# Performance work log

Hardware: AMD Instinct MI355X
Metric: run time of the kernel (lower is better)

Reference implementation:

```python
import jax, jax.numpy as jnp
import numpy as np

EMBED_DIM = 1024
NUM_HEADS = 16
HEAD_DIM = EMBED_DIM // NUM_HEADS
WINDOW = 256
B, S = 2, 2048


def setup_inputs() -> dict:
    key = jax.random.key(0)
    ks = jax.random.split(key, 9)
    sc = 1.0 / np.sqrt(EMBED_DIM)
    inp = {
        "x": jax.random.normal(ks[0], (B, S, EMBED_DIM), dtype=jnp.float32),
        "Wq": jax.random.normal(ks[1], (EMBED_DIM, EMBED_DIM), dtype=jnp.float32) * sc,
        "Wk": jax.random.normal(ks[2], (EMBED_DIM, EMBED_DIM), dtype=jnp.float32) * sc,
        "Wv": jax.random.normal(ks[3], (EMBED_DIM, EMBED_DIM), dtype=jnp.float32) * sc,
        "Wo": jax.random.normal(ks[4], (EMBED_DIM, EMBED_DIM), dtype=jnp.float32) * sc,
        "bq": jax.random.normal(ks[5], (EMBED_DIM,), dtype=jnp.float32) * 0.01,
        "bk": jax.random.normal(ks[6], (EMBED_DIM,), dtype=jnp.float32) * 0.01,
        "bv": jax.random.normal(ks[7], (EMBED_DIM,), dtype=jnp.float32) * 0.01,
        "bo": jax.random.normal(ks[8], (EMBED_DIM,), dtype=jnp.float32) * 0.01,
    }
    return inp


def _sliding_window_mask(seq_len: int) -> jnp.ndarray:
    # True where attention is NOT permitted (future or beyond window)
    idx = jnp.arange(seq_len)
    rel = idx[None, :] - idx[:, None]  # (S, S): key_pos - query_pos
    return (rel > 0) | (rel < -WINDOW)


def reference(x, Wq, Wk, Wv, Wo, bq, bk, bv, bo):
    Bx, Sx, E = x.shape
    H, D = NUM_HEADS, HEAD_DIM
    # projections (torch Linear: y = x @ W.T + b)
    q = (x @ Wq.T + bq).reshape(Bx, Sx, H, D).transpose(0, 2, 1, 3)  # (B,H,S,D)
    k = (x @ Wk.T + bk).reshape(Bx, Sx, H, D).transpose(0, 2, 1, 3)
    v = (x @ Wv.T + bv).reshape(Bx, Sx, H, D).transpose(0, 2, 1, 3)
    q = q * (D ** -0.5)
    attn = jnp.einsum("bhqd,bhkd->bhqk", q, k)  # (B,H,S,S) dense scores
    mask = _sliding_window_mask(Sx)
    attn = jnp.where(mask, -jnp.inf, attn)
    attn = jax.nn.softmax(attn, axis=-1)
    y = jnp.einsum("bhqk,bhkd->bhqd", attn, v)
    y = y.transpose(0, 2, 1, 3).reshape(Bx, Sx, E)
    return y @ Wo.T + bo
```

## Files before the change

kernel.cpp:

```cpp
#include <hip/hip_runtime.h>

#define E_DIM 1024
#define NHEAD 16
#define HDIM 64
#define SEQ 2048
#define NBATCH 2
#define WIN 256
#define MTOK (NBATCH * SEQ)
#define BKT 32
#define NT (E_DIM / BKT)

typedef __attribute__((ext_vector_type(4))) float f32x4;
typedef __attribute__((ext_vector_type(8))) short short8;
typedef __attribute__((ext_vector_type(4))) unsigned short u16x4;

#define AS1 __attribute__((address_space(1)))
#define AS3 __attribute__((address_space(3)))

__device__ __forceinline__ void gll16(const void* g, void* l) {
    __builtin_amdgcn_global_load_lds((const AS1 void*)g, (AS3 void*)l, 16, 0, 0);
}

__device__ __forceinline__ unsigned short f2bf(float f) {
    union { float f; unsigned u; } a; a.f = f;
    unsigned r = a.u + 0x7fffu + ((a.u >> 16) & 1u);
    return (unsigned short)(r >> 16);
}

__global__ __launch_bounds__(256) void conv_all(const float* __restrict__ x,
        const float* __restrict__ w0, const float* __restrict__ w1,
        const float* __restrict__ w2, const float* __restrict__ w3,
        unsigned short* __restrict__ xo,
        unsigned short* __restrict__ o0, unsigned short* __restrict__ o1,
        unsigned short* __restrict__ o2, unsigned short* __restrict__ o3) {
    const int seg = blockIdx.y;
    const float* src;
    unsigned short* dst;
    if (seg < 4) { src = x + (size_t)seg * 1048576; dst = xo + (size_t)seg * 1048576; }
    else {
        src = (seg == 4) ? w0 : (seg == 5) ? w1 : (seg == 6) ? w2 : w3;
        dst = (seg == 4) ? o0 : (seg == 5) ? o1 : (seg == 6) ? o2 : o3;
    }
    int i = blockIdx.x * 256 + threadIdx.x;
    float4 v = ((const float4*)src)[i];
    u16x4 o;
    o[0] = f2bf(v.x); o[1] = f2bf(v.y); o[2] = f2bf(v.z); o[3] = f2bf(v.w);
    ((u16x4*)dst)[i] = o;
}

__global__ __launch_bounds__(512, 2) void gemm8_qkv(const unsigned short* __restrict__ xb,
        const unsigned short* __restrict__ wqb, const unsigned short* __restrict__ wkb,
        const unsigned short* __restrict__ wvb,
        const float* __restrict__ bq, const float* __restrict__ bk, const float* __restrict__ bv,
        unsigned short* __restrict__ qo, unsigned short* __restrict__ ko,
        unsigned short* __restrict__ vTo) {
    __shared__ char lds[131072];
    const int tid = threadIdx.x;
    const int w = tid >> 6, l = tid & 63;
    const int r16 = l & 15, kq = l >> 4;
    const int wm = w >> 2, wn = w & 3;
    const int m0 = blockIdx.x * 256;
    const int by = blockIdx.y;
    const int mat = by >> 2;
    const int nb = (by & 3) * 256;
    const unsigned short* Bw = (mat == 0) ? wqb : (mat == 1) ? wkb : wvb;

    const int srow = tid >> 2;
    const int sslot = tid & 3;
    const int fsw = (srow >> 1) & 3;
    const int gslot = (sslot ^ fsw) * 8;
    const unsigned short* aSrc0 = xb + (size_t)(m0 + srow) * E_DIM + gslot;
    const unsigned short* aSrc1 = aSrc0 + (size_t)128 * E_DIM;
    const unsigned short* bSrc0 = Bw + (size_t)(nb + srow) * E_DIM + gslot;
    const unsigned short* bSrc1 = bSrc0 + (size_t)128 * E_DIM;
    const int dstOff = w * 1024;

#define STAGE_A(t) { char* d_ = lds + ((t) & 3) * 32768 + dstOff; \
                     gll16(aSrc0 + (t) * BKT, d_); gll16(aSrc1 + (t) * BKT, d_ + 8192); }
#define STAGE_B(t) { char* d_ = lds + ((t) & 3) * 32768 + 16384 + dstOff; \
                     gll16(bSrc0 + (t) * BKT, d_); gll16(bSrc1 + (t) * BKT, d_ + 8192); }

    f32x4 acc[8][4];
    #pragma unroll
    for (int m = 0; m < 8; ++m)
        #pragma unroll
        for (int n = 0; n < 4; ++n)
            acc[m][n] = (f32x4){0.f, 0.f, 0.f, 0.f};

    STAGE_A(0); STAGE_B(0); STAGE_A(1); STAGE_B(1);

    const int fs = (r16 >> 1) & 3;
    const int rdoff = (kq ^ fs) * 16;

    for (int t = 0; t < NT; ++t) {
        if (t < NT - 1) { asm volatile("s_waitcnt vmcnt(4)" ::: "memory"); }
        else            { asm volatile("s_waitcnt vmcnt(0)" ::: "memory"); }
        __builtin_amdgcn_sched_barrier(0);
        __builtin_amdgcn_s_barrier();
        __builtin_amdgcn_sched_barrier(0);
        char* la = lds + (t & 3) * 32768;
        char* lb = la + 16384;
        short8 bfr[4], af[8];
        #pragma unroll
        for (int n = 0; n < 4; ++n)
            bfr[n] = *(const short8*)(lb + (wn * 64 + n * 16 + r16) * 64 + rdoff);
        #pragma unroll
        for (int j = 0; j < 8; ++j)
            af[j] = *(const short8*)(la + (wm * 128 + j * 16 + r16) * 64 + rdoff);
        if (t + 2 < NT) { STAGE_A(t + 2); STAGE_B(t + 2); }
        __builtin_amdgcn_s_setprio(1);
        #pragma unroll
        for (int j = 0; j < 8; ++j)
            #pragma unroll
            for (int n = 0; n < 4; ++n)
                acc[j][n] = __builtin_amdgcn_mfma_f32_16x16x32_bf16(af[j], bfr[n], acc[j][n], 0, 0, 0);
        __builtin_amdgcn_s_setprio(0);
    }
#undef STAGE_A
#undef STAGE_B

    const float* bias = (mat == 0) ? bq : (mat == 1) ? bk : bv;
    const float scale = (mat == 0) ? 0.125f : 1.0f;
    #pragma unroll
    for (int n = 0; n < 4; ++n) {
        int e = nb + wn * 64 + n * 16 + r16;
        float bb = bias[e];
        int h = e >> 6, d = e & 63;
        #pragma unroll
        for (int m = 0; m < 8; ++m) {
            int tok = m0 + wm * 128 + m * 16 + kq * 4;
            int b = tok >> 11, s = tok & (SEQ - 1);
            if (mat == 2) {
                u16x4 o;
                #pragma unroll
                for (int r = 0; r < 4; ++r) o[r] = f2bf(acc[m][n][r] + bb);
                *(u16x4*)(vTo + ((size_t)(b * NHEAD + h) * HDIM + d) * SEQ + s) = o;
            } else {
                unsigned short* dst = (mat == 0) ? qo : ko;
                #pragma unroll
                for (int r = 0; r < 4; ++r) {
                    float val = (acc[m][n][r] + bb) * scale;
                    dst[((size_t)(b * NHEAD + h) * SEQ + s + r) * HDIM + d] = f2bf(val);
                }
            }
        }
    }
}

__global__ __launch_bounds__(256, 2) void gemm_out(const unsigned short* __restrict__ yb,
        const unsigned short* __restrict__ wob, const float* __restrict__ bo,
        float* __restrict__ out) {
    __shared__ char lds[65536];
    const int tid = threadIdx.x;
    const int w = tid >> 6, l = tid & 63;
    const int r16 = l & 15, kq = l >> 4;
    const int wr = w >> 1, wc = w & 1;
    const int m0 = blockIdx.x * 128;
    const int n0 = blockIdx.y * 128;

    const int srow = tid >> 2;
    const int sslot = tid & 3;
    const int fsw = (srow >> 1) & 3;
    const int gslot = (sslot ^ fsw) * 8;
    const unsigned short* aSrc0 = yb + (size_t)(m0 + srow) * E_DIM + gslot;
    const unsigned short* aSrc1 = aSrc0 + (size_t)64 * E_DIM;
    const unsigned short* bSrc0 = wob + (size_t)(n0 + srow) * E_DIM + gslot;
    const unsigned short* bSrc1 = bSrc0 + (size_t)64 * E_DIM;
    const int dstOff = w * 1024;

#define STAGE_A(t) { char* d_ = lds + ((t) & 3) * 16384 + dstOff; \
                     gll16(aSrc0 + (t) * BKT, d_); gll16(aSrc1 + (t) * BKT, d_ + 4096); }
#define STAGE_B(t) { char* d_ = lds + ((t) & 3) * 16384 + 8192 + dstOff; \
                     gll16(bSrc0 + (t) * BKT, d_); gll16(bSrc1 + (t) * BKT, d_ + 4096); }

    f32x4 acc[4][4];
    #pragma unroll
    for (int m = 0; m < 4; ++m)
        #pragma unroll
        for (int n = 0; n < 4; ++n)
            acc[m][n] = (f32x4){0.f, 0.f, 0.f, 0.f};

    STAGE_A(0); STAGE_B(0); STAGE_A(1); STAGE_B(1);

    const int fs = (r16 >> 1) & 3;
    const int rdoff = (kq ^ fs) * 16;

    for (int t = 0; t < NT; ++t) {
        if (t < NT - 1) { asm volatile("s_waitcnt vmcnt(4)" ::: "memory"); }
        else            { asm volatile("s_waitcnt vmcnt(0)" ::: "memory"); }
        __builtin_amdgcn_sched_barrier(0);
        __builtin_amdgcn_s_barrier();
        __builtin_amdgcn_sched_barrier(0);
        char* la = lds + (t & 3) * 16384;
        char* lb = la + 8192;
        short8 bfr[4], af[4];
        #pragma unroll
        for (int n = 0; n < 4; ++n)
            bfr[n] = *(const short8*)(lb + (wc * 64 + n * 16 + r16) * 64 + rdoff);
        #pragma unroll
        for (int m = 0; m < 4; ++m)
            af[m] = *(const short8*)(la + (wr * 64 + m * 16 + r16) * 64 + rdoff);
        if (t + 2 < NT) { STAGE_A(t + 2); STAGE_B(t + 2); }
        __builtin_amdgcn_s_setprio(1);
        #pragma unroll
        for (int m = 0; m < 4; ++m)
            #pragma unroll
            for (int n = 0; n < 4; ++n)
                acc[m][n] = __builtin_amdgcn_mfma_f32_16x16x32_bf16(af[m], bfr[n], acc[m][n], 0, 0, 0);
        __builtin_amdgcn_s_setprio(0);
    }
#undef STAGE_A
#undef STAGE_B

    #pragma unroll
    for (int n = 0; n < 4; ++n) {
        int e = n0 + wc * 64 + n * 16 + r16;
        float bb = bo[e];
        #pragma unroll
        for (int m = 0; m < 4; ++m) {
            #pragma unroll
            for (int r = 0; r < 4; ++r) {
                int tok = m0 + wr * 64 + m * 16 + kq * 4 + r;
                out[(size_t)tok * E_DIM + e] = acc[m][n][r] + bb;
            }
        }
    }
}

template<int MODE, bool PRE>
__device__ __forceinline__ void attn_tile(int k0,
        const unsigned short* __restrict__ kp, const unsigned short* __restrict__ vp,
        int r16, int kq, char* pl,
        const short8 (&qf)[2][2], short8 (&kf)[2][2],
        f32x4 (&po)[2][4], float (&mrow)[2][4], float (&lsum)[2][4]) {
    f32x4 sc[2][2];
    #pragma unroll
    for (int mf = 0; mf < 2; ++mf)
        #pragma unroll
        for (int n = 0; n < 2; ++n) {
            f32x4 z = {0.f, 0.f, 0.f, 0.f};
            z = __builtin_amdgcn_mfma_f32_16x16x32_bf16(qf[mf][0], kf[n][0], z, 0, 0, 0);
            sc[mf][n] = __builtin_amdgcn_mfma_f32_16x16x32_bf16(qf[mf][1], kf[n][1], z, 0, 0, 0);
        }
    if (PRE) {
        #pragma unroll
        for (int n = 0; n < 2; ++n) {
            const unsigned short* kr = kp + (size_t)(k0 + 32 + n * 16 + r16) * HDIM + kq * 8;
            kf[n][0] = *(const short8*)(kr);
            kf[n][1] = *(const short8*)(kr + 32);
        }
    }
    short8 vf[4];
    #pragma unroll
    for (int nn = 0; nn < 4; ++nn)
        vf[nn] = *(const short8*)(vp + (size_t)(nn * 16 + r16) * SEQ + k0 + kq * 8);

    float tmax[2][4];
    #pragma unroll
    for (int mf = 0; mf < 2; ++mf)
        #pragma unroll
        for (int r = 0; r < 4; ++r) {
            int rel = mf * 16 + kq * 4 + r;
            if (MODE == 1) {
                if (r16 < rel)      sc[mf][0][r] = -1e30f;
                if (16 + r16 < rel) sc[mf][1][r] = -1e30f;
            }
            if (MODE == 2) {
                if (r16 > rel)      sc[mf][0][r] = -1e30f;
                if (16 + r16 > rel) sc[mf][1][r] = -1e30f;
            }
            tmax[mf][r] = fmaxf(sc[mf][0][r], sc[mf][1][r]);
        }
    #pragma unroll
    for (int off = 1; off < 16; off <<= 1)
        #pragma unroll
        for (int mf = 0; mf < 2; ++mf)
            #pragma unroll
            for (int r = 0; r < 4; ++r)
                tmax[mf][r] = fmaxf(tmax[mf][r], __shfl_xor(tmax[mf][r], off));
    float pv[2][2][4];
    #pragma unroll
    for (int mf = 0; mf < 2; ++mf)
        #pragma unroll
        for (int r = 0; r < 4; ++r) {
            float mnew = fmaxf(mrow[mf][r], tmax[mf][r]);
            float resc = __expf(mrow[mf][r] - mnew);
            mrow[mf][r] = mnew;
            float p0 = __expf(sc[mf][0][r] - mnew);
            float p1 = __expf(sc[mf][1][r] - mnew);
            lsum[mf][r] = lsum[mf][r] * resc + p0 + p1;
            po[mf][0][r] *= resc; po[mf][1][r] *= resc;
            po[mf][2][r] *= resc; po[mf][3][r] *= resc;
            pv[mf][0][r] = p0; pv[mf][1][r] = p1;
        }
    #pragma unroll
    for (int mf = 0; mf < 2; ++mf)
        #pragma unroll
        for (int r = 0; r < 4; ++r) {
            int row = kq * 4 + r;
            int c0 = r16 ^ ((row & 7) << 3);
            int c1 = c0 ^ 16;
            *(unsigned short*)(pl + mf * 2048 + row * 128 + c0 * 2) = f2bf(pv[mf][0][r]);
            *(unsigned short*)(pl + mf * 2048 + row * 128 + c1 * 2) = f2bf(pv[mf][1][r]);
        }
    short8 pa[2];
    #pragma unroll
    for (int mf = 0; mf < 2; ++mf)
        pa[mf] = *(const short8*)(pl + mf * 2048 + r16 * 128 + ((kq ^ (r16 & 7)) * 16));
    #pragma unroll
    for (int nn = 0; nn < 4; ++nn) {
        po[0][nn] = __builtin_amdgcn_mfma_f32_16x16x32_bf16(pa[0], vf[nn], po[0][nn], 0, 0, 0);
        po[1][nn] = __builtin_amdgcn_mfma_f32_16x16x32_bf16(pa[1], vf[nn], po[1][nn], 0, 0, 0);
    }
}

__global__ __launch_bounds__(256) void attn_swa(const unsigned short* __restrict__ q,
                                                const unsigned short* __restrict__ k,
                                                const unsigned short* __restrict__ vT,
                                                unsigned short* __restrict__ y) {
    __shared__ char plds[4 * 4096];
    const int t = threadIdx.x;
    const int w = t >> 6, l = t & 63;
    const int r16 = l & 15, kq = l >> 4;
    const int wid = blockIdx.x * 4 + w;
    const int bh = wid >> 6;
    const int q0 = (wid & 63) * 32;
    const unsigned short* qp = q + (size_t)bh * SEQ * HDIM;
    const unsigned short* kp = k + (size_t)bh * SEQ * HDIM;
    const unsigned short* vp = vT + (size_t)bh * HDIM * SEQ;
    char* pl = plds + w * 4096;

    short8 qf[2][2];
    #pragma unroll
    for (int mf = 0; mf < 2; ++mf) {
        const unsigned short* qr = qp + (q0 + mf * 16 + r16) * HDIM + kq * 8;
        qf[mf][0] = *(const short8*)(qr);
        qf[mf][1] = *(const short8*)(qr + 32);
    }

    f32x4 po[2][4];
    float mrow[2][4], lsum[2][4];
    #pragma unroll
    for (int mf = 0; mf < 2; ++mf) {
        #pragma unroll
        for (int nn = 0; nn < 4; ++nn) po[mf][nn] = (f32x4){0.f, 0.f, 0.f, 0.f};
        #pragma unroll
        for (int r = 0; r < 4; ++r) { mrow[mf][r] = -1e30f; lsum[mf][r] = 0.f; }
    }

    const int kstart = (q0 >= WIN) ? (q0 - WIN) : 0;
    short8 kf[2][2];
    #pragma unroll
    for (int n = 0; n < 2; ++n) {
        const unsigned short* kr = kp + (size_t)(kstart + n * 16 + r16) * HDIM + kq * 8;
        kf[n][0] = *(const short8*)(kr);
        kf[n][1] = *(const short8*)(kr + 32);
    }

    int k0 = kstart;
    if (q0 >= WIN) {
        attn_tile<1, true>(k0, kp, vp, r16, kq, pl, qf, kf, po, mrow, lsum);
        k0 += 32;
    }
    for (; k0 < q0; k0 += 32)
        attn_tile<0, true>(k0, kp, vp, r16, kq, pl, qf, kf, po, mrow, lsum);
    attn_tile<2, false>(q0, kp, vp, r16, kq, pl, qf, kf, po, mrow, lsum);

    #pragma unroll
    for (int off = 1; off < 16; off <<= 1)
        #pragma unroll
        for (int mf = 0; mf < 2; ++mf)
            #pragma unroll
            for (int r = 0; r < 4; ++r)
                lsum[mf][r] += __shfl_xor(lsum[mf][r], off);

    const int b = bh >> 4, h = bh & 15;
    #pragma unroll
    for (int mf = 0; mf < 2; ++mf)
        #pragma unroll
        for (int nn = 0; nn < 4; ++nn)
            #pragma unroll
            for (int r = 0; r < 4; ++r) {
                int s = q0 + mf * 16 + kq * 4 + r;
                float val = po[mf][nn][r] / lsum[mf][r];
                y[((size_t)(b * SEQ + s)) * E_DIM + h * HDIM + nn * 16 + r16] = f2bf(val);
            }
}

extern "C" void kernel_launch(void* const* d_in, const int* in_sizes, int n_in,
                              void* d_out, int out_size, void* d_ws, size_t ws_size,
                              hipStream_t stream) {
    const float* x  = (const float*)d_in[0];
    const float* Wq = (const float*)d_in[1];
    const float* Wk = (const float*)d_in[2];
    const float* Wv = (const float*)d_in[3];
    const float* Wo = (const float*)d_in[4];
    const float* bq = (const float*)d_in[5];
    const float* bk = (const float*)d_in[6];
    const float* bv = (const float*)d_in[7];
    const float* bo = (const float*)d_in[8];
    float* out = (float*)d_out;

    char* ws = (char*)d_ws;
    unsigned short* xb  = (unsigned short*)(ws);
    unsigned short* wqb = (unsigned short*)(ws + ((size_t)8 << 20));
    unsigned short* wkb = (unsigned short*)(ws + ((size_t)10 << 20));
    unsigned short* wvb = (unsigned short*)(ws + ((size_t)12 << 20));
    unsigned short* wob = (unsigned short*)(ws + ((size_t)14 << 20));
    unsigned short* qw  = (unsigned short*)(ws + ((size_t)16 << 20));
    unsigned short* kw  = (unsigned short*)(ws + ((size_t)24 << 20));
    unsigned short* vTw = (unsigned short*)(ws + ((size_t)40 << 20));
    unsigned short* yw  = (unsigned short*)(ws + ((size_t)48 << 20));

    conv_all<<<dim3(1024, 8), 256, 0, stream>>>(x, Wq, Wk, Wv, Wo, xb, wqb, wkb, wvb, wob);

    gemm8_qkv<<<dim3(16, 12), 512, 0, stream>>>(xb, wqb, wkb, wvb, bq, bk, bv, qw, kw, vTw);
    attn_swa<<<512, 256, 0, stream>>>(qw, kw, vTw, yw);
    gemm_out<<<dim3(32, 8), 256, 0, stream>>>(yw, wob, bo, out);
}
```

Baseline: 162.2 us.

## Split QKV GEMM K-step into two halves interleaving LDS reads, staging and MFMA

The QKV projection GEMM main loop now splits each K-step into two phases. Phase one loads half of the A fragments, issues the A prefetch, and runs MFMAs. Phase two then loads the other half, issues the B prefetch, and runs the remaining MFMAs. The wait/barrier is moved to the end of the iteration, and a barrier plus lgkmcnt wait is added before compute, in both GEMM kernels. The aim is to overlap LDS reads and global-to-LDS staging with MFMA work and to cut register pressure from holding 8 A fragments at once. The cost is extra s_barriers per iteration.

```diff
diff --git a/kernel.cpp b/kernel.cpp
--- a/kernel.cpp
+++ b/kernel.cpp
@@ -88,33 +88,55 @@
             acc[m][n] = (f32x4){0.f, 0.f, 0.f, 0.f};
 
     STAGE_A(0); STAGE_B(0); STAGE_A(1); STAGE_B(1);
+    asm volatile("s_waitcnt vmcnt(4)" ::: "memory");
+    __builtin_amdgcn_sched_barrier(0);
+    __builtin_amdgcn_s_barrier();
 
     const int fs = (r16 >> 1) & 3;
     const int rdoff = (kq ^ fs) * 16;
 
     for (int t = 0; t < NT; ++t) {
-        if (t < NT - 1) { asm volatile("s_waitcnt vmcnt(4)" ::: "memory"); }
-        else            { asm volatile("s_waitcnt vmcnt(0)" ::: "memory"); }
-        __builtin_amdgcn_sched_barrier(0);
-        __builtin_amdgcn_s_barrier();
-        __builtin_amdgcn_sched_barrier(0);
         char* la = lds + (t & 3) * 32768;
         char* lb = la + 16384;
-        short8 bfr[4], af[8];
+        short8 bfr[4], af[4];
         #pragma unroll
         for (int n = 0; n < 4; ++n)
             bfr[n] = *(const short8*)(lb + (wn * 64 + n * 16 + r16) * 64 + rdoff);
         #pragma unroll
-        for (int j = 0; j < 8; ++j)
+        for (int j = 0; j < 4; ++j)
             af[j] = *(const short8*)(la + (wm * 128 + j * 16 + r16) * 64 + rdoff);
-        if (t + 2 < NT) { STAGE_A(t + 2); STAGE_B(t + 2); }
+        if (t + 2 < NT) STAGE_A(t + 2);
+        __builtin_amdgcn_s_barrier();
+        asm volatile("s_waitcnt lgkmcnt(0)" ::: "memory");
+        __builtin_amdgcn_sched_barrier(0);
         __builtin_amdgcn_s_setprio(1);
         #pragma unroll
-        for (int j = 0; j < 8; ++j)
+        for (int j = 0; j < 4; ++j)
             #pragma unroll
             for (int n = 0; n < 4; ++n)
                 acc[j][n] = __builtin_amdgcn_mfma_f32_16x16x32_bf16(af[j], bfr[n], acc[j][n], 0, 0, 0);
         __builtin_amdgcn_s_setprio(0);
+        short8 af2[4];
+        #pragma unroll
+        for (int j = 0; j < 4; ++j)
+            af2[j] = *(const short8*)(la + (wm * 128 + (4 + j) * 16 + r16) * 64 + rdoff);
+        if (t + 2 < NT) STAGE_B(t + 2);
+        __builtin_amdgcn_s_barrier();
+        asm volatile("s_waitcnt lgkmcnt(0)" ::: "memory");
+        __builtin_amdgcn_sched_barrier(0);
+        __builtin_amdgcn_s_setprio(1);
+        #pragma unroll
+        for (int j = 0; j < 4; ++j)
+            #pragma unroll
+            for (int n = 0; n < 4; ++n)
+                acc[4 + j][n] = __builtin_amdgcn_mfma_f32_16x16x32_bf16(af2[j], bfr[n], acc[4 + j][n], 0, 0, 0);
+        __builtin_amdgcn_s_setprio(0);
+        if (t < NT - 1) {
+            if (t < NT - 2) { asm volatile("s_waitcnt vmcnt(4)" ::: "memory"); }
+            else            { asm volatile("s_waitcnt vmcnt(0)" ::: "memory"); }
+            __builtin_amdgcn_sched_barrier(0);
+            __builtin_amdgcn_s_barrier();
+        }
     }
 #undef STAGE_A
 #undef STAGE_B
@@ -181,16 +203,14 @@
             acc[m][n] = (f32x4){0.f, 0.f, 0.f, 0.f};
 
     STAGE_A(0); STAGE_B(0); STAGE_A(1); STAGE_B(1);
+    asm volatile("s_waitcnt vmcnt(4)" ::: "memory");
+    __builtin_amdgcn_sched_barrier(0);
+    __builtin_amdgcn_s_barrier();
 
     const int fs = (r16 >> 1) & 3;
     const int rdoff = (kq ^ fs) * 16;
 
     for (int t = 0; t < NT; ++t) {
-        if (t < NT - 1) { asm volatile("s_waitcnt vmcnt(4)" ::: "memory"); }
-        else            { asm volatile("s_waitcnt vmcnt(0)" ::: "memory"); }
-        __builtin_amdgcn_sched_barrier(0);
-        __builtin_amdgcn_s_barrier();
-        __builtin_amdgcn_sched_barrier(0);
         char* la = lds + (t & 3) * 16384;
         char* lb = la + 8192;
         short8 bfr[4], af[4];
@@ -201,6 +221,9 @@
         for (int m = 0; m < 4; ++m)
             af[m] = *(const short8*)(la + (wr * 64 + m * 16 + r16) * 64 + rdoff);
         if (t + 2 < NT) { STAGE_A(t + 2); STAGE_B(t + 2); }
+        __builtin_amdgcn_s_barrier();
+        asm volatile("s_waitcnt lgkmcnt(0)" ::: "memory");
+        __builtin_amdgcn_sched_barrier(0);
         __builtin_amdgcn_s_setprio(1);
         #pragma unroll
         for (int m = 0; m < 4; ++m)
@@ -208,6 +231,12 @@
             for (int n = 0; n < 4; ++n)
                 acc[m][n] = __builtin_amdgcn_mfma_f32_16x16x32_bf16(af[m], bfr[n], acc[m][n], 0, 0, 0);
         __builtin_amdgcn_s_setprio(0);
+        if (t < NT - 1) {
+            if (t < NT - 2) { asm volatile("s_waitcnt vmcnt(4)" ::: "memory"); }
+            else            { asm volatile("s_waitcnt vmcnt(0)" ::: "memory"); }
+            __builtin_amdgcn_sched_barrier(0);
+            __builtin_amdgcn_s_barrier();
+        }
     }
 #undef STAGE_A
 #undef STAGE_B
```

Result: no change. 164.0 us (+1.1%).

## Shrink QKV GEMM tiles to 128x128 with double buffering, restructure out-GEMM barriers

Applied to the files above, without the earlier changes.

The QKV projection GEMM moves from 256x256 tiles with 512 threads and a 4-stage 128KB LDS ring to 128x128 tiles with 256 threads and a 2-stage 32KB double buffer, launching 768 blocks instead of 192. The goal is to fill all compute units on the MI355X with multiple resident blocks, since 192 blocks underfill the device. The output GEMM's barrier and waitcnt sequence moves to after the MFMA block, with an added LDS-read wait, so loads can overlap compute. The trade-offs are lower per-block data reuse, a simpler __syncthreads pipeline with less prefetch depth, and possible LDS race risk from the reordered barriers.

```diff
diff --git a/kernel.cpp b/kernel.cpp
--- a/kernel.cpp
+++ b/kernel.cpp
@@ -48,21 +48,21 @@
     ((u16x4*)dst)[i] = o;
 }
 
-__global__ __launch_bounds__(512, 2) void gemm8_qkv(const unsigned short* __restrict__ xb,
+__global__ __launch_bounds__(256, 3) void gemm97_qkv(const unsigned short* __restrict__ xb,
         const unsigned short* __restrict__ wqb, const unsigned short* __restrict__ wkb,
         const unsigned short* __restrict__ wvb,
         const float* __restrict__ bq, const float* __restrict__ bk, const float* __restrict__ bv,
         unsigned short* __restrict__ qo, unsigned short* __restrict__ ko,
         unsigned short* __restrict__ vTo) {
-    __shared__ char lds[131072];
+    __shared__ char lds[32768];
     const int tid = threadIdx.x;
     const int w = tid >> 6, l = tid & 63;
     const int r16 = l & 15, kq = l >> 4;
-    const int wm = w >> 2, wn = w & 3;
-    const int m0 = blockIdx.x * 256;
+    const int wr = w >> 1, wc = w & 1;
+    const int m0 = blockIdx.x * 128;
     const int by = blockIdx.y;
-    const int mat = by >> 2;
-    const int nb = (by & 3) * 256;
+    const int mat = by >> 3;
+    const int nb = (by & 7) * 128;
     const unsigned short* Bw = (mat == 0) ? wqb : (mat == 1) ? wkb : wvb;
 
     const int srow = tid >> 2;
@@ -70,65 +70,60 @@
     const int fsw = (srow >> 1) & 3;
     const int gslot = (sslot ^ fsw) * 8;
     const unsigned short* aSrc0 = xb + (size_t)(m0 + srow) * E_DIM + gslot;
-    const unsigned short* aSrc1 = aSrc0 + (size_t)128 * E_DIM;
+    const unsigned short* aSrc1 = aSrc0 + (size_t)64 * E_DIM;
     const unsigned short* bSrc0 = Bw + (size_t)(nb + srow) * E_DIM + gslot;
-    const unsigned short* bSrc1 = bSrc0 + (size_t)128 * E_DIM;
+    const unsigned short* bSrc1 = bSrc0 + (size_t)64 * E_DIM;
     const int dstOff = w * 1024;
 
-#define STAGE_A(t) { char* d_ = lds + ((t) & 3) * 32768 + dstOff; \
-                     gll16(aSrc0 + (t) * BKT, d_); gll16(aSrc1 + (t) * BKT, d_ + 8192); }
-#define STAGE_B(t) { char* d_ = lds + ((t) & 3) * 32768 + 16384 + dstOff; \
-                     gll16(bSrc0 + (t) * BKT, d_); gll16(bSrc1 + (t) * BKT, d_ + 8192); }
-
-    f32x4 acc[8][4];
-    #pragma unroll
-    for (int m = 0; m < 8; ++m)
+#define STAGE(t) { char* a_ = lds + ((t) & 1) * 16384 + dstOff; \
+                   char* b_ = a_ + 8192; \
+                   gll16(aSrc0 + (t) * BKT, a_); gll16(aSrc1 + (t) * BKT, a_ + 4096); \
+                   gll16(bSrc0 + (t) * BKT, b_); gll16(bSrc1 + (t) * BKT, b_ + 4096); }
+
+    f32x4 acc[4][4];
+    #pragma unroll
+    for (int m = 0; m < 4; ++m)
         #pragma unroll
         for (int n = 0; n < 4; ++n)
             acc[m][n] = (f32x4){0.f, 0.f, 0.f, 0.f};
 
-    STAGE_A(0); STAGE_B(0); STAGE_A(1); STAGE_B(1);
+    STAGE(0);
 
     const int fs = (r16 >> 1) & 3;
     const int rdoff = (kq ^ fs) * 16;
 
     for (int t = 0; t < NT; ++t) {
-        if (t < NT - 1) { asm volatile("s_waitcnt vmcnt(4)" ::: "memory"); }
-        else            { asm volatile("s_waitcnt vmcnt(0)" ::: "memory"); }
-        __builtin_amdgcn_sched_barrier(0);
-        __builtin_amdgcn_s_barrier();
-        __builtin_amdgcn_sched_barrier(0);
-        char* la = lds + (t & 3) * 32768;
-        char* lb = la + 16384;
-        short8 bfr[4], af[8];
+        __syncthreads();
+        if (t + 1 < NT) STAGE(t + 1);
+        char* la = lds + (t & 1) * 16384;
+        char* lb = la + 8192;
+        short8 af[4], bfr[4];
+        #pragma unroll
+        for (int m = 0; m < 4; ++m)
+            af[m] = *(const short8*)(la + (wr * 64 + m * 16 + r16) * 64 + rdoff);
         #pragma unroll
         for (int n = 0; n < 4; ++n)
-            bfr[n] = *(const short8*)(lb + (wn * 64 + n * 16 + r16) * 64 + rdoff);
-        #pragma unroll
-        for (int j = 0; j < 8; ++j)
-            af[j] = *(const short8*)(la + (wm * 128 + j * 16 + r16) * 64 + rdoff);
-        if (t + 2 < NT) { STAGE_A(t + 2); STAGE_B(t + 2); }
+            bfr[n] = *(const short8*)(lb + (wc * 64 + n * 16 + r16) * 64 + rdoff);
         __builtin_amdgcn_s_setprio(1);
         #pragma unroll
-        for (int j = 0; j < 8; ++j)
+        for (int m = 0; m < 4; ++m)
             #pragma unroll
             for (int n = 0; n < 4; ++n)
-                acc[j][n] = __builtin_amdgcn_mfma_f32_16x16x32_bf16(af[j], bfr[n], acc[j][n], 0, 0, 0);
+                acc[m][n] = __builtin_amdgcn_mfma_f32_16x16x32_bf16(af[m], bfr[n], acc[m][n], 0, 0, 0);
         __builtin_amdgcn_s_setprio(0);
     }
-#undef STAGE_A
-#undef STAGE_B
+#undef STAGE
 
     const float* bias = (mat == 0) ? bq : (mat == 1) ? bk : bv;
     const float scale = (mat == 0) ? 0.125f : 1.0f;
     #pragma unroll
     for (int n = 0; n < 4; ++n) {
-        int e = nb + wn * 64 + n * 16 + r16;
+        int e = nb + wc * 64 + n * 16 + r16;
         float bb = bias[e];
         int h = e >> 6, d = e & 63;
         #pragma unroll
-        for (int m = 0; m < 8; ++m) {
-            int tok = m0 + wm * 128 + m * 16 + kq * 4;
+        for (int m = 0; m < 4; ++m) {
+            int tok = m0 + wr * 64 + m * 16 + kq * 4;
             int b = tok >> 11, s = tok & (SEQ - 1);
             if (mat == 2) {
                 u16x4 o;
@@ -181,16 +176,14 @@
             acc[m][n] = (f32x4){0.f, 0.f, 0.f, 0.f};
 
     STAGE_A(0); STAGE_B(0); STAGE_A(1); STAGE_B(1);
+    asm volatile("s_waitcnt vmcnt(4)" ::: "memory");
+    __builtin_amdgcn_sched_barrier(0);
+    __builtin_amdgcn_s_barrier();
 
     const int fs = (r16 >> 1) & 3;
     const int rdoff = (kq ^ fs) * 16;
 
     for (int t = 0; t < NT; ++t) {
-        if (t < NT - 1) { asm volatile("s_waitcnt vmcnt(4)" ::: "memory"); }
-        else            { asm volatile("s_waitcnt vmcnt(0)" ::: "memory"); }
-        __builtin_amdgcn_sched_barrier(0);
-        __builtin_amdgcn_s_barrier();
-        __builtin_amdgcn_sched_barrier(0);
         char* la = lds + (t & 3) * 16384;
         char* lb = la + 8192;
         short8 bfr[4], af[4];
@@ -201,6 +194,9 @@
         for (int m = 0; m < 4; ++m)
             af[m] = *(const short8*)(la + (wr * 64 + m * 16 + r16) * 64 + rdoff);
         if (t + 2 < NT) { STAGE_A(t + 2); STAGE_B(t + 2); }
+        __builtin_amdgcn_s_barrier();
+        asm volatile("s_waitcnt lgkmcnt(0)" ::: "memory");
+        __builtin_amdgcn_sched_barrier(0);
         __builtin_amdgcn_s_setprio(1);
         #pragma unroll
         for (int m = 0; m < 4; ++m)
@@ -208,6 +204,12 @@
             for (int n = 0; n < 4; ++n)
                 acc[m][n] = __builtin_amdgcn_mfma_f32_16x16x32_bf16(af[m], bfr[n], acc[m][n], 0, 0, 0);
         __builtin_amdgcn_s_setprio(0);
+        if (t < NT - 1) {
+            if (t < NT - 2) { asm volatile("s_waitcnt vmcnt(4)" ::: "memory"); }
+            else            { asm volatile("s_waitcnt vmcnt(0)" ::: "memory"); }
+            __builtin_amdgcn_sched_barrier(0);
+            __builtin_amdgcn_s_barrier();
+        }
     }
 #undef STAGE_A
 #undef STAGE_B
@@ -414,7 +416,7 @@
 
     conv_all<<<dim3(1024, 8), 256, 0, stream>>>(x, Wq, Wk, Wv, Wo, xb, wqb, wkb, wvb, wob);
 
-    gemm8_qkv<<<dim3(16, 12), 512, 0, stream>>>(xb, wqb, wkb, wvb, bq, bk, bv, qw, kw, vTw);
+    gemm97_qkv<<<dim3(32, 24), 256, 0, stream>>>(xb, wqb, wkb, wvb, bq, bk, bv, qw, kw, vTw);
     attn_swa<<<512, 256, 0, stream>>>(qw, kw, vTw, yw);
     gemm_out<<<dim3(32, 8), 256, 0, stream>>>(yw, wob, bo, out);
 }
```

Result: no change. 164.0 us (+1.1%).
